# Performance work log

Measured on AMD Instinct MI355X. Metric: run time of the kernel, lower is better.

The kernel has to match this reference:

```python
import jax, jax.numpy as jnp
import numpy as np

N_EMBD = 1024
N_HEAD = 16
HEAD_DIM = N_EMBD // N_HEAD


def setup_inputs() -> dict:
    key = jax.random.key(0)
    ks = jax.random.split(key, 8)
    B, T, T_ctx, C = 2, 2048, 2048, N_EMBD
    s = 1.0 / np.sqrt(C)
    return {
        "x": jax.random.normal(ks[0], (B, T, C), dtype=jnp.float32),
        "context": jax.random.normal(ks[1], (B, T_ctx, C), dtype=jnp.float32),
        # Linear weights stored as [in, out] (torch stores [out, in]; math identical via x @ W)
        "Wq": jax.random.normal(ks[2], (C, C), dtype=jnp.float32) * s,
        "bq": jnp.zeros((C,), dtype=jnp.float32),
        "Wkv": jax.random.normal(ks[3], (C, 2 * C), dtype=jnp.float32) * s,
        "bkv": jnp.zeros((2 * C,), dtype=jnp.float32),
        "Wp": jax.random.normal(ks[4], (C, C), dtype=jnp.float32) * s,
        "bp": jnp.zeros((C,), dtype=jnp.float32),
    }


def reference(x, context, Wq, bq, Wkv, bkv, Wp, bp):
    B, T, C = x.shape
    T_ctx = context.shape[1]
    H, D = N_HEAD, C // N_HEAD

    q = (x @ Wq + bq).reshape(B, T, H, D).transpose(0, 2, 1, 3)          # [B,H,T,D]
    kv = context @ Wkv + bkv                                             # [B,T_ctx,2C]
    k, v = jnp.split(kv, 2, axis=-1)
    k = k.reshape(B, T_ctx, H, D).transpose(0, 2, 1, 3)                  # [B,H,T_ctx,D]
    v = v.reshape(B, T_ctx, H, D).transpose(0, 2, 1, 3)                  # [B,H,T_ctx,D]

    att = jnp.einsum("bhtd,bhsd->bhts", q, k) * (1.0 / jnp.sqrt(jnp.asarray(D, q.dtype)))
    # tril(ones(T, T_ctx)): position t attends to context positions s <= t
    causal = jnp.arange(T)[:, None] >= jnp.arange(T_ctx)[None, :]        # [T,T_ctx]
    att = jnp.where(causal[None, None], att, jnp.asarray(-jnp.inf, att.dtype))
    att = jax.nn.softmax(att, axis=-1)

    y = jnp.einsum("bhts,bhsd->bhtd", att, v)                            # [B,H,T,D]
    y = y.transpose(0, 2, 1, 3).reshape(B, T, C)
    return y @ Wp + bp
```

## Files before the change

### kernel.cpp

```cpp
#include <hip/hip_runtime.h>
#include <hip/hip_bf16.h>

typedef __bf16 bf16;
typedef __bf16 bf16x8 __attribute__((ext_vector_type(8)));
typedef __bf16 bf16x4 __attribute__((ext_vector_type(4)));
typedef float f32x4 __attribute__((ext_vector_type(4)));
typedef float f32x16 __attribute__((ext_vector_type(16)));

#define GLOAD_LDS16(g, l) \
  __builtin_amdgcn_global_load_lds((const __attribute__((address_space(1))) void*)(g), \
                                   (__attribute__((address_space(3))) void*)(l), 16, 0, 0)

static __device__ __forceinline__ unsigned cvtpk_bf16(float lo, float hi) {
  unsigned r;
  asm("v_cvt_pk_bf16_f32 %0, %1, %2" : "=v"(r) : "v"(lo), "v"(hi));
  return r;
}
static __device__ __forceinline__ void pl32swap(unsigned& a, unsigned& b) {
  asm volatile("v_permlane32_swap_b32 %0, %1" : "+v"(a), "+v"(b));
}

__global__ __launch_bounds__(256) void prep_kernel(
    const float* __restrict__ x, const float* __restrict__ ctx,
    const float* __restrict__ Wq, const float* __restrict__ Wkv, const float* __restrict__ Wp,
    bf16* __restrict__ x_bf, bf16* __restrict__ c_bf,
    bf16* __restrict__ Wq_t, bf16* __restrict__ Wkv_t, bf16* __restrict__ Wp_t) {
  const int bid = blockIdx.x;
  if (bid < 8192) {
    const int i = (bid & 4095) * 256 + threadIdx.x;
    const float4 v = (bid < 4096) ? ((const float4*)x)[i] : ((const float4*)ctx)[i];
    bf16x4 o;
    o.x = (bf16)v.x; o.y = (bf16)v.y; o.z = (bf16)v.z; o.w = (bf16)v.w;
    if (bid < 4096) ((bf16x4*)x_bf)[i] = o; else ((bf16x4*)c_bf)[i] = o;
    return;
  }
  __shared__ float tile[32][33];
  int tb = bid - 8192;
  const float* W; bf16* Wt; int N;
  if (tb < 1024) { W = Wq; Wt = Wq_t; N = 1024; }
  else if (tb < 3072) { W = Wkv; Wt = Wkv_t; N = 2048; tb -= 1024; }
  else { W = Wp; Wt = Wp_t; N = 1024; tb -= 3072; }
  const int nt = N >> 5;
  const int n0 = (tb % nt) * 32, k0 = (tb / nt) * 32;
  const int tx = threadIdx.x & 31, ty = threadIdx.x >> 5;
#pragma unroll
  for (int i = 0; i < 32; i += 8)
    tile[ty + i][tx] = W[(size_t)(k0 + ty + i) * N + n0 + tx];
  __syncthreads();
#pragma unroll
  for (int i = 0; i < 32; i += 8)
    Wt[(size_t)(n0 + ty + i) * 1024 + k0 + tx] = (bf16)tile[tx][ty + i];
}

__global__ __launch_bounds__(256, 4) void proj_gemm_kernel(
    const bf16* __restrict__ x_bf, const bf16* __restrict__ c_bf,
    const bf16* __restrict__ Wq_t, const bf16* __restrict__ Wkv_t,
    const float* __restrict__ bq, const float* __restrict__ bkv,
    bf16* __restrict__ Qh, bf16* __restrict__ Kh, bf16* __restrict__ Vt) {
  __shared__ __align__(16) bf16 SM[16384];
  bf16* As = SM;
  bf16* Bs = SM + 8192;
  bf16* Vb = SM;

  const int tid = threadIdx.x;
  const int lane = tid & 63;
  const int w = tid >> 6;
  const int wr = w >> 1, wc = w & 1;
  const int g4 = lane >> 4, r16 = lane & 15;
  const int wu = __builtin_amdgcn_readfirstlane(w);

  int bid = blockIdx.x;
  bid = (bid & 7) * 96 + (bid >> 3);
  const bool isq = bid < 256;
  const int lid = isq ? bid : bid - 256;
  const int bx = isq ? (lid & 7) : (lid & 15);
  const int by = isq ? (lid >> 3) : (lid >> 4);
  const int m0 = by * 128, n0 = bx * 128;
  const bf16* A = isq ? x_bf : c_bf;
  const bf16* Bt = isq ? Wq_t : Wkv_t;
  const float* bias = isq ? bq : bkv;

  const bf16* Abase = A + (size_t)m0 * 1024;
  const bf16* Bbase = Bt + (size_t)n0 * 1024;
  int aoff[4];
#pragma unroll
  for (int it = 0; it < 4; ++it) {
    const int s = it * 256 + tid;
    const int row = s >> 3, j = s & 7;
    const int jj = j ^ (row & 7);
    aoff[it] = row * 1024 + jj * 8;
  }

  f32x4 acc[4][4] = {};

  for (int k0 = 0; k0 < 1024; k0 += 64) {
    __syncthreads();
#pragma unroll
    for (int it = 0; it < 4; ++it) {
      GLOAD_LDS16(Abase + aoff[it] + k0, As + (it * 256 + wu * 64) * 8);
      GLOAD_LDS16(Bbase + aoff[it] + k0, Bs + (it * 256 + wu * 64) * 8);
    }
    __syncthreads();
#pragma unroll
    for (int kk = 0; kk < 2; ++kk) {
      bf16x8 af[4], bfr[4];
#pragma unroll
      for (int i = 0; i < 4; i++) {
        const int lr = wr * 64 + i * 16 + r16;
        af[i] = *(const bf16x8*)(As + lr * 64 + ((kk * 4 + g4) ^ (lr & 7)) * 8);
      }
#pragma unroll
      for (int i = 0; i < 4; i++) {
        const int lr = wc * 64 + i * 16 + r16;
        bfr[i] = *(const bf16x8*)(Bs + lr * 64 + ((kk * 4 + g4) ^ (lr & 7)) * 8);
      }
#pragma unroll
      for (int mi = 0; mi < 4; mi++)
#pragma unroll
        for (int ni = 0; ni < 4; ni++)
          acc[mi][ni] = __builtin_amdgcn_mfma_f32_16x16x32_bf16(af[mi], bfr[ni], acc[mi][ni], 0, 0, 0);
    }
  }

  if (!isq && n0 >= 1024) {
    const int bb = m0 >> 11, t0l = m0 & 2047;
#pragma unroll
    for (int p = 0; p < 2; ++p) {
      __syncthreads();
      if (wc == p) {
#pragma unroll
        for (int mi = 0; mi < 4; mi++)
#pragma unroll
          for (int ni = 0; ni < 4; ni++) {
            const int cl = ni * 16 + r16;
            const float bv = bias[n0 + p * 64 + cl];
#pragma unroll
            for (int r = 0; r < 4; r++) {
              const int rl = wr * 64 + mi * 16 + 4 * g4 + r;
              Vb[cl * 128 + rl] = (bf16)(acc[mi][ni][r] + bv);
            }
          }
      }
      __syncthreads();
      const int c2 = n0 - 1024 + p * 64;
#pragma unroll
      for (int pp = 0; pp < 4; ++pp) {
        const int slot = tid + pp * 256;
        const int d = slot >> 4, j = slot & 15;
        const int cc = c2 + d;
        const int h = cc >> 6, dd = cc & 63;
        *(bf16x8*)(Vt + ((size_t)((bb * 16 + h) * 64 + dd)) * 2048 + t0l + j * 8) =
            *(const bf16x8*)(Vb + d * 128 + j * 8);
      }
    }
    return;
  }

#pragma unroll
  for (int mi = 0; mi < 4; mi++) {
#pragma unroll
    for (int ni = 0; ni < 4; ni++) {
      const int col = n0 + wc * 64 + ni * 16 + r16;
      const float bv = bias[col];
      const int rowb = m0 + wr * 64 + mi * 16 + 4 * g4;
      const int h = col >> 6, d = col & 63;
#pragma unroll
      for (int r = 0; r < 4; r++) {
        const int row = rowb + r;
        const int bb = row >> 11, t = row & 2047;
        const float v = acc[mi][ni][r] + bv;
        if (isq)
          Qh[((size_t)(bb * 16 + h) * 2048 + t) * 64 + d] = (bf16)(v * 0.18033688f);
        else
          Kh[((size_t)(bb * 16 + h) * 2048 + t) * 64 + d] = (bf16)v;
      }
    }
  }
}

__global__ __launch_bounds__(256) void gemm_out_kernel(
    const bf16* __restrict__ A, const bf16* __restrict__ Bt,
    const float* __restrict__ bias, float* __restrict__ out) {
  __shared__ __align__(16) bf16 As[128 * 64];
  __shared__ __align__(16) bf16 Bs[64 * 64];

  const int tid = threadIdx.x;
  const int lane = tid & 63;
  const int w = tid >> 6;
  const int wr = w >> 1, wc = w & 1;
  const int g4 = lane >> 4, r16 = lane & 15;
  const int wu = __builtin_amdgcn_readfirstlane(w);

  int bid = blockIdx.x;
  bid = (bid & 7) * 64 + (bid >> 3);
  const int bx = bid & 15, by = bid >> 4;
  const int m0 = by * 128, n0 = bx * 64;

  const bf16* Abase = A + (size_t)m0 * 1024;
  const bf16* Bbase = Bt + (size_t)n0 * 1024;
  int aoff[4], boff[2];
#pragma unroll
  for (int it = 0; it < 4; ++it) {
    const int s = it * 256 + tid;
    const int row = s >> 3, j = s & 7;
    aoff[it] = row * 1024 + (j ^ (row & 7)) * 8;
  }
#pragma unroll
  for (int it = 0; it < 2; ++it) {
    const int s = it * 256 + tid;
    const int row = s >> 3, j = s & 7;
    boff[it] = row * 1024 + (j ^ (row & 7)) * 8;
  }

  f32x4 acc[4][2] = {};

  for (int k0 = 0; k0 < 1024; k0 += 64) {
    __syncthreads();
#pragma unroll
    for (int it = 0; it < 4; ++it)
      GLOAD_LDS16(Abase + aoff[it] + k0, As + (it * 256 + wu * 64) * 8);
#pragma unroll
    for (int it = 0; it < 2; ++it)
      GLOAD_LDS16(Bbase + boff[it] + k0, Bs + (it * 256 + wu * 64) * 8);
    __syncthreads();
#pragma unroll
    for (int kk = 0; kk < 2; ++kk) {
      bf16x8 af[4], bfr[2];
#pragma unroll
      for (int i = 0; i < 4; i++) {
        const int lr = wr * 64 + i * 16 + r16;
        af[i] = *(const bf16x8*)(As + lr * 64 + ((kk * 4 + g4) ^ (lr & 7)) * 8);
      }
#pragma unroll
      for (int i = 0; i < 2; i++) {
        const int lr = wc * 32 + i * 16 + r16;
        bfr[i] = *(const bf16x8*)(Bs + lr * 64 + ((kk * 4 + g4) ^ (lr & 7)) * 8);
      }
#pragma unroll
      for (int mi = 0; mi < 4; mi++)
#pragma unroll
        for (int ni = 0; ni < 2; ni++)
          acc[mi][ni] = __builtin_amdgcn_mfma_f32_16x16x32_bf16(af[mi], bfr[ni], acc[mi][ni], 0, 0, 0);
    }
  }

#pragma unroll
  for (int mi = 0; mi < 4; mi++)
#pragma unroll
    for (int ni = 0; ni < 2; ni++) {
      const int col = n0 + wc * 32 + ni * 16 + r16;
      const float bv = bias[col];
      const int rowb = m0 + wr * 64 + mi * 16 + 4 * g4;
#pragma unroll
      for (int r = 0; r < 4; r++)
        out[(size_t)(rowb + r) * 1024 + col] = acc[mi][ni][r] + bv;
    }
}

#define AE2(c, tb, te, sl) ((c) | ((tb) << 3) | ((te) << 9) | ((sl) << 15))
__constant__ int ATAB[12] = {
  AE2(7, 0, 16, 6), AE2(7, 16, 32, 7), AE2(3, 0, 16, 0),
  AE2(6, 0, 14, 4), AE2(6, 14, 28, 5), AE2(5, 0, 12, 2),
  AE2(5, 12, 24, 3), AE2(2, 0, 12, 0), AE2(4, 0, 10, 0),
  AE2(4, 10, 20, 1), AE2(1, 0, 8, 0),  AE2(0, 0, 4, 0),
};

__global__ __launch_bounds__(512) void attn_kernel(
    const bf16* __restrict__ Q, const bf16* __restrict__ Kh,
    const bf16* __restrict__ Vt, bf16* __restrict__ Y,
    bf16* __restrict__ Po, float* __restrict__ Lsum) {
  __shared__ __align__(16) bf16 Kls[2][4096];
  __shared__ __align__(16) bf16 Vls[2][4096];

  const int tid = threadIdx.x;
  const int lane = tid & 63;
  const int w = tid >> 6;
  const int l31 = lane & 31;
  const int g = lane >> 5;
  const int u = blockIdx.x >> 5;
  const int bh = blockIdx.x & 31;
  const int e = ATAB[u];
  const int c = e & 7, tb = (e >> 3) & 63, te = (e >> 9) & 63, slot = (e >> 15) & 7;
  const int slotg = bh * 8 + slot;
  const bool single = (tb == 0) && (te == 4 * c + 4);
  const int b = bh >> 4, h = bh & 15;
  const int qb = c * 256;
  const int wq = qb + w * 32;
  const int wu = __builtin_amdgcn_readfirstlane(w);

  bf16x8 qf[4];
  {
    const bf16* qp = Q + ((size_t)bh * 2048 + wq + l31) * 64 + g * 8;
#pragma unroll
    for (int cc = 0; cc < 4; ++cc) qf[cc] = *(const bf16x8*)(qp + cc * 16);
  }

  f32x16 O0 = {}, O1 = {};
  float l = 0.f;

  auto stage = [&](int bi, int s0) {
    const int s = tid >> 3, j = tid & 7;
    const int js = (j ^ (s & 7)) * 8;
    GLOAD_LDS16(Kh + ((size_t)bh * 2048 + s0 + s) * 64 + js, &Kls[bi][wu * 512]);
    GLOAD_LDS16(Vt + ((size_t)bh * 64 + s) * 2048 + s0 + js, &Vls[bi][wu * 512]);
  };

  stage(tb & 1, tb * 64);

  for (int t = tb; t < te; ++t) {
    const int s0 = t * 64;
    asm volatile("s_waitcnt vmcnt(0)" ::: "memory");
    __builtin_amdgcn_s_barrier();
    asm volatile("" ::: "memory");
    if (t + 1 < te) stage((t + 1) & 1, s0 + 64);

    if (s0 < wq + 32) {
      const bf16* Kb = Kls[t & 1];
      const bf16* Vb = Vls[t & 1];

      f32x16 SA = {}, SB = {};
      __builtin_amdgcn_s_setprio(1);
#pragma unroll
      for (int cc = 0; cc < 4; ++cc) {
        const int sl = ((cc * 2 + g) ^ (l31 & 7)) * 8;
        bf16x8 kf0 = *(const bf16x8*)(Kb + l31 * 64 + sl);
        SA = __builtin_amdgcn_mfma_f32_32x32x16_bf16(kf0, qf[cc], SA, 0, 0, 0);
        bf16x8 kf1 = *(const bf16x8*)(Kb + (32 + l31) * 64 + sl);
        SB = __builtin_amdgcn_mfma_f32_32x32x16_bf16(kf1, qf[cc], SB, 0, 0, 0);
      }
      __builtin_amdgcn_s_setprio(0);

      const int qg = wq + l31;
      if (s0 + 63 > wq) {
#pragma unroll
        for (int r = 0; r < 16; ++r) {
          const int sl = (r & 3) + 8 * (r >> 2) + 4 * g;
          SA[r] = (s0 + sl <= qg) ? SA[r] : -3.0e38f;
          SB[r] = (s0 + 32 + sl <= qg) ? SB[r] : -3.0e38f;
        }
      }

      float ps = 0.f;
#pragma unroll
      for (int r = 0; r < 16; ++r) { SA[r] = __builtin_amdgcn_exp2f(SA[r]); ps += SA[r]; }
#pragma unroll
      for (int r = 0; r < 16; ++r) { SB[r] = __builtin_amdgcn_exp2f(SB[r]); ps += SB[r]; }
      l += ps;

      union PW { unsigned u[4]; bf16x8 v; };
      PW pa0, pa1, pa2, pa3;
      {
        unsigned A0 = cvtpk_bf16(SA[0], SA[1]), B0 = cvtpk_bf16(SA[2], SA[3]);
        unsigned C0 = cvtpk_bf16(SA[4], SA[5]), D0 = cvtpk_bf16(SA[6], SA[7]);
        pl32swap(A0, C0); pl32swap(B0, D0);
        pa0.u[0] = A0; pa0.u[1] = B0; pa0.u[2] = C0; pa0.u[3] = D0;

        unsigned A1 = cvtpk_bf16(SA[8], SA[9]), B1 = cvtpk_bf16(SA[10], SA[11]);
        unsigned C1 = cvtpk_bf16(SA[12], SA[13]), D1 = cvtpk_bf16(SA[14], SA[15]);
        pl32swap(A1, C1); pl32swap(B1, D1);
        pa1.u[0] = A1; pa1.u[1] = B1; pa1.u[2] = C1; pa1.u[3] = D1;

        unsigned A2 = cvtpk_bf16(SB[0], SB[1]), B2 = cvtpk_bf16(SB[2], SB[3]);
        unsigned C2 = cvtpk_bf16(SB[4], SB[5]), D2 = cvtpk_bf16(SB[6], SB[7]);
        pl32swap(A2, C2); pl32swap(B2, D2);
        pa2.u[0] = A2; pa2.u[1] = B2; pa2.u[2] = C2; pa2.u[3] = D2;

        unsigned A3 = cvtpk_bf16(SB[8], SB[9]), B3 = cvtpk_bf16(SB[10], SB[11]);
        unsigned C3 = cvtpk_bf16(SB[12], SB[13]), D3 = cvtpk_bf16(SB[14], SB[15]);
        pl32swap(A3, C3); pl32swap(B3, D3);
        pa3.u[0] = A3; pa3.u[1] = B3; pa3.u[2] = C3; pa3.u[3] = D3;
      }

      __builtin_amdgcn_s_setprio(1);
#pragma unroll
      for (int cc = 0; cc < 4; ++cc) {
        const bf16x8 pav = (cc == 0) ? pa0.v : (cc == 1) ? pa1.v : (cc == 2) ? pa2.v : pa3.v;
        const int sl = ((cc * 2 + g) ^ (l31 & 7)) * 8;
        bf16x8 vf0 = *(const bf16x8*)(Vb + l31 * 64 + sl);
        O0 = __builtin_amdgcn_mfma_f32_32x32x16_bf16(pav, vf0, O0, 0, 0, 0);
        bf16x8 vf1 = *(const bf16x8*)(Vb + (32 + l31) * 64 + sl);
        O1 = __builtin_amdgcn_mfma_f32_32x32x16_bf16(pav, vf1, O1, 0, 0, 0);
      }
      __builtin_amdgcn_s_setprio(0);
    }
  }

  l += __shfl_xor(l, 32, 64);
  if (!single && g == 0)
    Lsum[(size_t)slotg * 256 + w * 32 + l31] = l;
#pragma unroll
  for (int r = 0; r < 16; ++r) {
    const int qr = (r & 3) + 8 * (r >> 2) + (g << 2);
    const float lr = __shfl(l, qr, 64);
    const float inv = (lr > 0.f) ? 1.f / lr : 0.f;
    if (single) {
      const int tq = wq + qr;
      bf16* yp = Y + ((size_t)(b * 2048 + tq)) * 1024 + h * 64 + l31;
      yp[0]  = (bf16)(O0[r] * inv);
      yp[32] = (bf16)(O1[r] * inv);
    } else {
      bf16* pp = Po + (size_t)slotg * 16384 + (w * 32 + qr) * 64 + l31;
      pp[0]  = (bf16)(O0[r] * inv);
      pp[32] = (bf16)(O1[r] * inv);
    }
  }
}

__global__ __launch_bounds__(256) void attn_combine(
    const bf16* __restrict__ Po, const float* __restrict__ Lsum, bf16* __restrict__ Y) {
  const int bh = blockIdx.x >> 2, ci = blockIdx.x & 3;
  const int c = ci + 4;
  const int base = bh * 8 + ci * 2;
  const int b = bh >> 4, h = bh & 15;
  const int tid = threadIdx.x;
#pragma unroll
  for (int k = 0; k < 8; ++k) {
    const int tt = tid + k * 256;
    const int row = tt >> 3, cg = tt & 7;
    const float w0 = Lsum[(size_t)base * 256 + row];
    const float w1 = Lsum[(size_t)(base + 1) * 256 + row];
    const bf16x8 v0 = *(const bf16x8*)(Po + (size_t)base * 16384 + row * 64 + cg * 8);
    const bf16x8 v1 = *(const bf16x8*)(Po + (size_t)(base + 1) * 16384 + row * 64 + cg * 8);
    const float inv = 1.f / (w0 + w1);
    bf16x8 o;
#pragma unroll
    for (int j = 0; j < 8; ++j) o[j] = (bf16)((w0 * (float)v0[j] + w1 * (float)v1[j]) * inv);
    const int t = c * 256 + row;
    *(bf16x8*)(Y + ((size_t)(b * 2048 + t)) * 1024 + h * 64 + cg * 8) = o;
  }
}

extern "C" void kernel_launch(void* const* d_in, const int* in_sizes, int n_in,
                              void* d_out, int out_size, void* d_ws, size_t ws_size,
                              hipStream_t stream) {
  (void)in_sizes; (void)n_in; (void)out_size; (void)ws_size;
  const float* x   = (const float*)d_in[0];
  const float* ctx = (const float*)d_in[1];
  const float* Wq  = (const float*)d_in[2];
  const float* bq  = (const float*)d_in[3];
  const float* Wkv = (const float*)d_in[4];
  const float* bkv = (const float*)d_in[5];
  const float* Wp  = (const float*)d_in[6];
  const float* bp  = (const float*)d_in[7];
  float* out = (float*)d_out;

  char* ws = (char*)d_ws;
  const size_t MB = 1024 * 1024;
  bf16*  Po    = (bf16*)(ws + 0 * MB);
  float* Lsum  = (float*)(ws + 9 * MB);
  bf16* x_bf   = (bf16*)(ws + 0 * MB);
  bf16* c_bf   = (bf16*)(ws + 10 * MB);
  bf16* Wq_t   = (bf16*)(ws + 18 * MB);
  bf16* Wkv_t  = (bf16*)(ws + 20 * MB);
  bf16* Wp_t   = (bf16*)(ws + 24 * MB);
  bf16* Qh     = (bf16*)(ws + 26 * MB);
  bf16* Kh     = (bf16*)(ws + 34 * MB);
  bf16* Vt     = (bf16*)(ws + 42 * MB);
  bf16* y_bf   = (bf16*)(ws + 50 * MB);

  prep_kernel<<<12288, 256, 0, stream>>>(x, ctx, Wq, Wkv, Wp, x_bf, c_bf, Wq_t, Wkv_t, Wp_t);
  proj_gemm_kernel<<<768, 256, 0, stream>>>(x_bf, c_bf, Wq_t, Wkv_t, bq, bkv, Qh, Kh, Vt);
  attn_kernel<<<384, 512, 0, stream>>>(Qh, Kh, Vt, y_bf, Po, Lsum);
  attn_combine<<<128, 256, 0, stream>>>(Po, Lsum, y_bf);
  gemm_out_kernel<<<512, 256, 0, stream>>>(y_bf, Wp_t, bp, out);
}
```

Measured before the change: 101.4 us.

## Enlarge projection GEMM tile to 256x128 with 8 waves per block

The Q/KV projection GEMM now uses 512-thread blocks computing 256x128 output tiles, with 8 waves arranged 2x4, each owning a 128x32 sub-tile. It launches half as many blocks and loads less B data per output element. The V-transpose epilogue staging buffer is padded to a 264 stride to fit the taller tile. The trade-off is more LDS per block and fewer blocks to fill the 256 CUs, which may lower occupancy and latency hiding.

Result: faster. 97.86 us (-3.5%).

```diff
diff --git a/kernel.cpp b/kernel.cpp
--- a/kernel.cpp
+++ b/kernel.cpp
@@ -52,73 +52,76 @@
     Wt[(size_t)(n0 + ty + i) * 1024 + k0 + tx] = (bf16)tile[tx][ty + i];
 }
 
-__global__ __launch_bounds__(256, 4) void proj_gemm_kernel(
+__global__ __launch_bounds__(512) void proj_gemm_kernel(
     const bf16* __restrict__ x_bf, const bf16* __restrict__ c_bf,
     const bf16* __restrict__ Wq_t, const bf16* __restrict__ Wkv_t,
     const float* __restrict__ bq, const float* __restrict__ bkv,
     bf16* __restrict__ Qh, bf16* __restrict__ Kh, bf16* __restrict__ Vt) {
-  __shared__ __align__(16) bf16 SM[16384];
+  __shared__ __align__(16) bf16 SM[24576];
   bf16* As = SM;
-  bf16* Bs = SM + 8192;
+  bf16* Bs = SM + 16384;
   bf16* Vb = SM;
 
   const int tid = threadIdx.x;
   const int lane = tid & 63;
   const int w = tid >> 6;
-  const int wr = w >> 1, wc = w & 1;
+  const int wm = w >> 2, wn = w & 3;
   const int g4 = lane >> 4, r16 = lane & 15;
   const int wu = __builtin_amdgcn_readfirstlane(w);
 
   int bid = blockIdx.x;
-  bid = (bid & 7) * 96 + (bid >> 3);
-  const bool isq = bid < 256;
-  const int lid = isq ? bid : bid - 256;
+  bid = (bid & 7) * 48 + (bid >> 3);
+  const bool isq = bid < 128;
+  const int lid = isq ? bid : bid - 128;
   const int bx = isq ? (lid & 7) : (lid & 15);
   const int by = isq ? (lid >> 3) : (lid >> 4);
-  const int m0 = by * 128, n0 = bx * 128;
+  const int m0 = by * 256, n0 = bx * 128;
   const bf16* A = isq ? x_bf : c_bf;
   const bf16* Bt = isq ? Wq_t : Wkv_t;
   const float* bias = isq ? bq : bkv;
 
   const bf16* Abase = A + (size_t)m0 * 1024;
   const bf16* Bbase = Bt + (size_t)n0 * 1024;
-  int aoff[4];
+  int aoff[4], boff[2];
 #pragma unroll
   for (int it = 0; it < 4; ++it) {
-    const int s = it * 256 + tid;
+    const int s = it * 512 + tid;
     const int row = s >> 3, j = s & 7;
-    const int jj = j ^ (row & 7);
-    aoff[it] = row * 1024 + jj * 8;
-  }
-
-  f32x4 acc[4][4] = {};
+    aoff[it] = row * 1024 + (j ^ (row & 7)) * 8;
+  }
+#pragma unroll
+  for (int it = 0; it < 2; ++it) {
+    const int s = it * 512 + tid;
+    const int row = s >> 3, j = s & 7;
+    boff[it] = row * 1024 + (j ^ (row & 7)) * 8;
+  }
+
+  f32x4 acc[8][2] = {};
 
   for (int k0 = 0; k0 < 1024; k0 += 64) {
     __syncthreads();
 #pragma unroll
-    for (int it = 0; it < 4; ++it) {
-      GLOAD_LDS16(Abase + aoff[it] + k0, As + (it * 256 + wu * 64) * 8);
-      GLOAD_LDS16(Bbase + aoff[it] + k0, Bs + (it * 256 + wu * 64) * 8);
-    }
+    for (int it = 0; it < 4; ++it)
+      GLOAD_LDS16(Abase + aoff[it] + k0, As + (it * 512 + wu * 64) * 8);
+#pragma unroll
+    for (int it = 0; it < 2; ++it)
+      GLOAD_LDS16(Bbase + boff[it] + k0, Bs + (it * 512 + wu * 64) * 8);
     __syncthreads();
 #pragma unroll
     for (int kk = 0; kk < 2; ++kk) {
-      bf16x8 af[4], bfr[4];
-#pragma unroll
-      for (int i = 0; i < 4; i++) {
-        const int lr = wr * 64 + i * 16 + r16;
-        af[i] = *(const bf16x8*)(As + lr * 64 + ((kk * 4 + g4) ^ (lr & 7)) * 8);
-      }
-#pragma unroll
-      for (int i = 0; i < 4; i++) {
-        const int lr = wc * 64 + i * 16 + r16;
-        bfr[i] = *(const bf16x8*)(Bs + lr * 64 + ((kk * 4 + g4) ^ (lr & 7)) * 8);
-      }
-#pragma unroll
-      for (int mi = 0; mi < 4; mi++)
-#pragma unroll
-        for (int ni = 0; ni < 4; ni++)
-          acc[mi][ni] = __builtin_amdgcn_mfma_f32_16x16x32_bf16(af[mi], bfr[ni], acc[mi][ni], 0, 0, 0);
+      bf16x8 bfr[2];
+#pragma unroll
+      for (int ni = 0; ni < 2; ni++) {
+        const int lr = wn * 32 + ni * 16 + r16;
+        bfr[ni] = *(const bf16x8*)(Bs + lr * 64 + ((kk * 4 + g4) ^ (lr & 7)) * 8);
+      }
+#pragma unroll
+      for (int mi = 0; mi < 8; mi++) {
+        const int lr = wm * 128 + mi * 16 + r16;
+        const bf16x8 a = *(const bf16x8*)(As + lr * 64 + ((kk * 4 + g4) ^ (lr & 7)) * 8);
+        acc[mi][0] = __builtin_amdgcn_mfma_f32_16x16x32_bf16(a, bfr[0], acc[mi][0], 0, 0, 0);
+        acc[mi][1] = __builtin_amdgcn_mfma_f32_16x16x32_bf16(a, bfr[1], acc[mi][1], 0, 0, 0);
+      }
     }
   }
 
@@ -127,42 +130,42 @@
 #pragma unroll
     for (int p = 0; p < 2; ++p) {
       __syncthreads();
-      if (wc == p) {
-#pragma unroll
-        for (int mi = 0; mi < 4; mi++)
-#pragma unroll
-          for (int ni = 0; ni < 4; ni++) {
-            const int cl = ni * 16 + r16;
+      if ((wn >> 1) == p) {
+#pragma unroll
+        for (int mi = 0; mi < 8; mi++)
+#pragma unroll
+          for (int ni = 0; ni < 2; ni++) {
+            const int cl = (wn & 1) * 32 + ni * 16 + r16;
             const float bv = bias[n0 + p * 64 + cl];
 #pragma unroll
             for (int r = 0; r < 4; r++) {
-              const int rl = wr * 64 + mi * 16 + 4 * g4 + r;
-              Vb[cl * 128 + rl] = (bf16)(acc[mi][ni][r] + bv);
+              const int rl = wm * 128 + mi * 16 + 4 * g4 + r;
+              Vb[cl * 264 + rl] = (bf16)(acc[mi][ni][r] + bv);
             }
           }
       }
       __syncthreads();
-      const int c2 = n0 - 1024 + p * 64;
+      const int c2b = n0 - 1024 + p * 64;
 #pragma unroll
       for (int pp = 0; pp < 4; ++pp) {
-        const int slot = tid + pp * 256;
-        const int d = slot >> 4, j = slot & 15;
-        const int cc = c2 + d;
+        const int slot = tid + pp * 512;
+        const int d = slot >> 5, j = slot & 31;
+        const int cc = c2b + d;
         const int h = cc >> 6, dd = cc & 63;
         *(bf16x8*)(Vt + ((size_t)((bb * 16 + h) * 64 + dd)) * 2048 + t0l + j * 8) =
-            *(const bf16x8*)(Vb + d * 128 + j * 8);
+            *(const bf16x8*)(Vb + d * 264 + j * 8);
       }
     }
     return;
   }
 
 #pragma unroll
-  for (int mi = 0; mi < 4; mi++) {
-#pragma unroll
-    for (int ni = 0; ni < 4; ni++) {
-      const int col = n0 + wc * 64 + ni * 16 + r16;
+  for (int mi = 0; mi < 8; mi++) {
+#pragma unroll
+    for (int ni = 0; ni < 2; ni++) {
+      const int col = n0 + wn * 32 + ni * 16 + r16;
       const float bv = bias[col];
-      const int rowb = m0 + wr * 64 + mi * 16 + 4 * g4;
+      const int rowb = m0 + wm * 128 + mi * 16 + 4 * g4;
       const int h = col >> 6, d = col & 63;
 #pragma unroll
       for (int r = 0; r < 4; r++) {
@@ -459,7 +462,7 @@
   bf16* y_bf   = (bf16*)(ws + 50 * MB);
 
   prep_kernel<<<12288, 256, 0, stream>>>(x, ctx, Wq, Wkv, Wp, x_bf, c_bf, Wq_t, Wkv_t, Wp_t);
-  proj_gemm_kernel<<<768, 256, 0, stream>>>(x_bf, c_bf, Wq_t, Wkv_t, bq, bkv, Qh, Kh, Vt);
+  proj_gemm_kernel<<<384, 512, 0, stream>>>(x_bf, c_bf, Wq_t, Wkv_t, bq, bkv, Qh, Kh, Vt);
   attn_kernel<<<384, 512, 0, stream>>>(Qh, Kh, Vt, y_bf, Po, Lsum);
   attn_combine<<<128, 256, 0, stream>>>(Po, Lsum, y_bf);
   gemm_out_kernel<<<512, 256, 0, stream>>>(y_bf, Wp_t, bp, out);
```
